# Optimization experiments

Hardware: AMD Instinct MI355X
Metric: run time of the kernel (lower is better)

## Reference

```python
import jax, jax.numpy as jnp
import numpy as np

B, T, C, NH = 8, 512, 512, 8
HD = C // NH

def _layernorm(x, g, b, eps=1e-5):
    mu = jnp.mean(x, axis=-1, keepdims=True)
    var = jnp.var(x, axis=-1, keepdims=True)
    return (x - mu) * jax.lax.rsqrt(var + eps) * g + b

def setup_inputs() -> dict:
    key = jax.random.key(0)
    ks = jax.random.split(key, 5)
    return {
        "x": jax.random.normal(ks[0], (B, T, C), jnp.float32),
        "w_attn": jax.random.normal(ks[1], (3 * C, C), jnp.float32) * (1.0 / np.sqrt(C)),
        "b_attn": jnp.zeros((3 * C,), jnp.float32),
        "w_proj": jax.random.normal(ks[2], (C, C), jnp.float32) * (1.0 / np.sqrt(C)),
        "b_proj": jnp.zeros((C,), jnp.float32),
        "q_gamma": jnp.ones((C,), jnp.float32),
        "q_beta": jnp.zeros((C,), jnp.float32),
        "k_gamma": jnp.ones((C,), jnp.float32),
        "k_beta": jnp.zeros((C,), jnp.float32),
        "rel_emb": jax.random.normal(ks[3], (T, C), jnp.float32) * 0.02,
    }

def reference(x, w_attn, b_attn, w_proj, b_proj, q_gamma, q_beta, k_gamma, k_beta, rel_emb):
    b, t, c = x.shape
    # QKV projection (torch Linear: x @ W.T + b)
    qkv = x @ w_attn.T + b_attn                       # [B,T,3C]
    q, k, v = jnp.split(qkv, 3, axis=-1)
    # per-stream LayerNorm over full embedding dim (q_ln/k_ln = LayerNorm(n_embd))
    q = _layernorm(q, q_gamma, q_beta)
    k = _layernorm(k, k_gamma, k_beta)
    # split heads -> [B,NH,T,HD]
    q = q.reshape(b, t, NH, HD).transpose(0, 2, 1, 3)
    k = k.reshape(b, t, NH, HD).transpose(0, 2, 1, 3)
    v = v.reshape(b, t, NH, HD).transpose(0, 2, 1, 3)
    # relative-position bias: gather rel_emb[|i-j|] -> [T,T,NH,HD]
    idx = jnp.abs(jnp.arange(t)[None, :] - jnp.arange(t)[:, None])  # [T,T] int
    rel = rel_emb[idx].reshape(t, t, NH, HD)
    rel_bias = jnp.einsum("bhqd,qkhd->bhqk", q, rel)  # [B,NH,T,T]
    scale = 1.0 / np.sqrt(HD)
    scores = (jnp.einsum("bhqd,bhkd->bhqk", q, k) + rel_bias) * scale
    causal = jnp.tril(jnp.ones((t, t), bool))
    scores = jnp.where(causal[None, None], scores, jnp.finfo(scores.dtype).min)
    att = jax.nn.softmax(scores, axis=-1)
    y = jnp.einsum("bhqk,bhkd->bhqd", att, v)         # [B,NH,T,HD]
    y = y.transpose(0, 2, 1, 3).reshape(b, t, c)
    return y @ w_proj.T + b_proj
```

## Files before the change

### kernel.cpp

```cpp
#include <hip/hip_runtime.h>
#include <hip/hip_bf16.h>
#include <cstddef>

#define BB 8
#define TT 512
#define CC 512
#define NHH 8
#define HDD 64

typedef __attribute__((ext_vector_type(8))) short short8;
typedef __attribute__((ext_vector_type(4))) float f32x4;

__device__ __forceinline__ unsigned short f2bf(float f) {
    unsigned u = __float_as_uint(f);
    u += 0x7FFFu + ((u >> 16) & 1u);
    return (unsigned short)(u >> 16);
}
__device__ __forceinline__ float bf2f(unsigned short h) {
    return __uint_as_float(((unsigned)h) << 16);
}

__global__ __launch_bounds__(256) void cvt_all_k(
    const float* __restrict__ x, const float* __restrict__ wa,
    const float* __restrict__ wp, const float* __restrict__ rel,
    unsigned short* __restrict__ Xb, unsigned short* __restrict__ Wqb,
    unsigned short* __restrict__ Wpb, unsigned short* __restrict__ Relb)
{
    const int bidx = blockIdx.x;
    const float* in;
    unsigned short* out;
    int base;
    if (bidx < 2048)      { in = x;   out = Xb;   base = bidx; }
    else if (bidx < 2816) { in = wa;  out = Wqb;  base = bidx - 2048; }
    else if (bidx < 3072) { in = wp;  out = Wpb;  base = bidx - 2816; }
    else                  { in = rel; out = Relb; base = bidx - 3072; }
    const int i = base * 1024 + threadIdx.x * 4;
    const float4 v = *(const float4*)(in + i);
    unsigned short tmp[4] = {f2bf(v.x), f2bf(v.y), f2bf(v.z), f2bf(v.w)};
    *(uint2*)(out + i) = *(const uint2*)tmp;
}

__global__ __launch_bounds__(256, 2) void gemm_qkv_mfma(
    const unsigned short* __restrict__ Xb, const unsigned short* __restrict__ Wb,
    const float* __restrict__ bias, unsigned short* __restrict__ qkbuf,
    unsigned short* __restrict__ VT)
{
    __shared__ __align__(16) unsigned short lds[128 * 136];

    const int tid = threadIdx.x;
    const int w = tid >> 6, lane = tid & 63;
    const int c = lane & 15, quad = lane >> 4;
    const int wm = w >> 1, wn = w & 1;
    const int bm = blockIdx.y * 128, bn = blockIdx.x * 128;

    const unsigned short* pp[8];
#pragma unroll
    for (int l = 0; l < 8; ++l) {
        const int ci = w * 8 + l;
        if (ci < 16) {
            const int m16 = ci >> 1, kk = ci & 1;
            pp[l] = Xb + (size_t)(bm + m16 * 16 + c) * 512 + kk * 32 + quad * 8;
        } else {
            const int cb = ci - 16, n16 = cb >> 1, kk = cb & 1;
            pp[l] = Wb + (size_t)(bn + n16 * 16 + c) * 512 + kk * 32 + quad * 8;
        }
    }

    f32x4 acc[4][4];
#pragma unroll
    for (int i = 0; i < 4; ++i)
#pragma unroll
        for (int j = 0; j < 4; ++j) acc[i][j] = (f32x4){0.f, 0.f, 0.f, 0.f};

    short8 pre[8];
#pragma unroll
    for (int l = 0; l < 8; ++l) pre[l] = *(const short8*)pp[l];

    for (int k0 = 0; k0 < 512; k0 += 64) {
        __syncthreads();
#pragma unroll
        for (int l = 0; l < 8; ++l)
            *(short8*)&lds[(w * 8 + l) * 512 + lane * 8] = pre[l];
        __syncthreads();
        if (k0 + 64 < 512) {
#pragma unroll
            for (int l = 0; l < 8; ++l)
                pre[l] = *(const short8*)(pp[l] + k0 + 64);
        }
#pragma unroll
        for (int kk = 0; kk < 2; ++kk) {
            short8 af[4], bfr[4];
#pragma unroll
            for (int i = 0; i < 4; ++i)
                af[i] = *(const short8*)&lds[((wm * 4 + i) * 2 + kk) * 512 + lane * 8];
#pragma unroll
            for (int j = 0; j < 4; ++j)
                bfr[j] = *(const short8*)&lds[(16 + (wn * 4 + j) * 2 + kk) * 512 + lane * 8];
#pragma unroll
            for (int i = 0; i < 4; ++i)
#pragma unroll
                for (int j = 0; j < 4; ++j)
                    acc[i][j] = __builtin_amdgcn_mfma_f32_16x16x32_bf16(
                        af[i], bfr[j], acc[i][j], 0, 0, 0);
        }
    }

    float bj[4];
#pragma unroll
    for (int j = 0; j < 4; ++j) bj[j] = bias[bn + wn * 64 + j * 16 + c];

    if (bn < 1024) {
#pragma unroll
        for (int i = 0; i < 4; ++i)
#pragma unroll
            for (int j = 0; j < 4; ++j) {
                const int n = bn + wn * 64 + j * 16 + c;
#pragma unroll
                for (int r = 0; r < 4; ++r) {
                    const int m = bm + wm * 64 + i * 16 + quad * 4 + r;
                    qkbuf[(size_t)m * 1024 + n] = f2bf(acc[i][j][r] + bj[j]);
                }
            }
    } else {
        __syncthreads();
#pragma unroll
        for (int i = 0; i < 4; ++i)
#pragma unroll
            for (int j = 0; j < 4; ++j) {
                const int col = wn * 64 + j * 16 + c;
                const int row0 = wm * 64 + i * 16 + quad * 4;
                unsigned short t4[4];
#pragma unroll
                for (int r = 0; r < 4; ++r) t4[r] = f2bf(acc[i][j][r] + bj[j]);
                *(uint2*)&lds[col * 136 + row0] = *(const uint2*)t4;
            }
        __syncthreads();
        const int bi = bm >> 9, tb = bm & 511;
        const int hd0 = bn - 1024;
#pragma unroll
        for (int l = 0; l < 8; ++l) {
            const int idx = l * 256 + tid;
            const int col = idx >> 4, grp = idx & 15;
            const short8 v = *(const short8*)&lds[col * 136 + grp * 8];
            const int hd = hd0 + col, h = hd >> 6, d = hd & 63;
            *(short8*)(VT + ((size_t)(bi * NHH + h) * HDD + d) * TT + tb + grp * 8) = v;
        }
    }
}

__global__ __launch_bounds__(256) void ln_k(
    const unsigned short* __restrict__ qkbuf,
    const float* __restrict__ qg, const float* __restrict__ qb,
    const float* __restrict__ kg, const float* __restrict__ kb,
    unsigned short* __restrict__ Qh, unsigned short* __restrict__ Kh)
{
    const int wv = threadIdx.x >> 6, lane = threadIdx.x & 63;
    const int row = blockIdx.x * 4 + wv;
    const int bi = row >> 9, t = row & 511;
    const unsigned short* base = qkbuf + (size_t)row * 1024;

#pragma unroll
    for (int s = 0; s < 2; ++s) {
        const short8 v8 = *(const short8*)(base + s * 512 + lane * 8);
        float vf[8];
#pragma unroll
        for (int i = 0; i < 8; ++i) vf[i] = bf2f(((const unsigned short*)&v8)[i]);
        float sum = 0.f, sq = 0.f;
#pragma unroll
        for (int i = 0; i < 8; ++i) { sum += vf[i]; sq += vf[i] * vf[i]; }
#pragma unroll
        for (int off = 1; off < 64; off <<= 1) {
            sum += __shfl_xor(sum, off);
            sq += __shfl_xor(sq, off);
        }
        const float mu = sum * (1.f / 512.f);
        const float var = sq * (1.f / 512.f) - mu * mu;
        const float rsg = rsqrtf(var + 1e-5f);
        const float* gam = (s ? kg : qg) + lane * 8;
        const float* bet = (s ? kb : qb) + lane * 8;
        const float4 g0 = *(const float4*)gam, g1 = *(const float4*)(gam + 4);
        const float4 b0 = *(const float4*)bet, b1 = *(const float4*)(bet + 4);
        const float gv[8] = {g0.x, g0.y, g0.z, g0.w, g1.x, g1.y, g1.z, g1.w};
        const float bv[8] = {b0.x, b0.y, b0.z, b0.w, b1.x, b1.y, b1.z, b1.w};
        unsigned short o8[8];
#pragma unroll
        for (int i = 0; i < 8; ++i)
            o8[i] = f2bf((vf[i] - mu) * rsg * gv[i] + bv[i]);
        unsigned short* outp = s ? Kh : Qh;
        *(short8*)(outp + ((size_t)(bi * NHH + (lane >> 3)) * TT + t) * HDD
                   + (lane & 7) * 8) = *(const short8*)o8;
    }
}

#define RD_BODY(nr_)                                                            \
    {                                                                           \
        const short8 br0 = *(const short8*)&Rels[((nr_) * 2 + 0) * 512 + lane * 8]; \
        const short8 br1 = *(const short8*)&Rels[((nr_) * 2 + 1) * 512 + lane * 8]; \
        f32x4 a2 = (f32x4){0.f, 0.f, 0.f, 0.f};                                 \
        a2 = __builtin_amdgcn_mfma_f32_16x16x32_bf16(aq0, br0, a2, 0, 0, 0);    \
        a2 = __builtin_amdgcn_mfma_f32_16x16x32_bf16(aq1, br1, a2, 0, 0, 0);    \
        const int colw = (mbase + (nr_) * 16 + c) & 127;                        \
        _Pragma("unroll")                                                       \
        for (int r = 0; r < 4; ++r)                                             \
            RDs[w][(quad * 4 + r) * 132 + colw] = f2bf(a2[r]);                  \
    }

__global__ __launch_bounds__(256, 2) void attn_k(
    const unsigned short* __restrict__ Qh, const unsigned short* __restrict__ Kh,
    const unsigned short* __restrict__ VT, const unsigned short* __restrict__ Relb,
    unsigned short* __restrict__ Yb)
{
    __shared__ __align__(16) unsigned short Qs[8 * 512];
    __shared__ __align__(16) unsigned short Ks[8 * 512];
    __shared__ __align__(16) unsigned short Vs[8 * 512];
    __shared__ __align__(16) unsigned short Rels[16 * 512];
    __shared__ __align__(16) unsigned short Ps[4][16 * 72];
    __shared__ __align__(16) unsigned short RDs[4][16 * 132];

    const int tid = threadIdx.x;
    const int w = tid >> 6;
    const int lane = tid & 63;
    const int c = lane & 15;
    const int quad = lane >> 4;

    const int bid = blockIdx.x;
    const int bit0 = bid & 1, bit8 = (bid >> 8) & 1;
    const int s_ = bit0 ^ bit8;
    const int q0 = (bid >> 1) & 7;
    const int qt = s_ ? 7 - q0 : q0;
    const int h = (bid >> 4) & 7;
    const int b = ((bid >> 7) & 1) | (bit8 << 1) | (bit0 << 2);
    const int i0 = qt * 64;

    const unsigned short* Qbase = Qh + (size_t)(b * NHH + h) * TT * HDD;
    const unsigned short* Kbase = Kh + (size_t)(b * NHH + h) * TT * HDD;
    const unsigned short* Vbase = VT + (size_t)(b * NHH + h) * HDD * TT;
    const unsigned short* Rbase = Relb + h * HDD;

#pragma unroll
    for (int kk = 0; kk < 2; ++kk) {
        const unsigned short* gp =
            Qbase + (size_t)(i0 + w * 16 + c) * HDD + kk * 32 + quad * 8;
        *(short8*)&Qs[(w * 2 + kk) * 512 + lane * 8] = *(const short8*)gp;
    }

    f32x4 oacc[4];
    float m_i[4], l_i[4];
#pragma unroll
    for (int r = 0; r < 4; ++r) { m_i[r] = -1e30f; l_i[r] = 0.f; }
#pragma unroll
    for (int nd = 0; nd < 4; ++nd) oacc[nd] = (f32x4){0.f, 0.f, 0.f, 0.f};

    short8 aq0, aq1;

    for (int jt = 0; jt <= qt; ++jt) {
        const int j0 = jt * 64;
#pragma unroll
        for (int kk = 0; kk < 2; ++kk) {
            const unsigned short* gp =
                Kbase + (size_t)(j0 + w * 16 + c) * HDD + kk * 32 + quad * 8;
            *(short8*)&Ks[(w * 2 + kk) * 512 + lane * 8] = *(const short8*)gp;
        }
#pragma unroll
        for (int js = 0; js < 2; ++js) {
            const unsigned short* gp =
                Vbase + (size_t)(w * 16 + c) * TT + j0 + js * 32 + quad * 8;
            *(short8*)&Vs[(w * 2 + js) * 512 + lane * 8] = *(const short8*)gp;
        }
        const int mbase = i0 - j0 - 63;
        if (jt == 0) {
#pragma unroll
            for (int sb = 0; sb < 2; ++sb) {
#pragma unroll
                for (int kk = 0; kk < 2; ++kk) {
                    const int n16 = w * 2 + sb;
                    int mrow = mbase + n16 * 16 + c;
                    mrow = mrow < 0 ? 0 : (mrow > 511 ? 511 : mrow);
                    *(short8*)&Rels[(n16 * 2 + kk) * 512 + lane * 8] =
                        *(const short8*)(Rbase + (size_t)mrow * CC + kk * 32 + quad * 8);
                }
            }
        } else {
#pragma unroll
            for (int kk = 0; kk < 2; ++kk) {
                int mrow = mbase + w * 16 + c;
                mrow = mrow < 0 ? 0 : (mrow > 511 ? 511 : mrow);
                *(short8*)&Rels[(w * 2 + kk) * 512 + lane * 8] =
                    *(const short8*)(Rbase + (size_t)mrow * CC + kk * 32 + quad * 8);
            }
        }
        __syncthreads();

        if (jt == 0) {
            aq0 = *(const short8*)&Qs[(w * 2 + 0) * 512 + lane * 8];
            aq1 = *(const short8*)&Qs[(w * 2 + 1) * 512 + lane * 8];
        }

        f32x4 sAcc[4];
#pragma unroll
        for (int ns = 0; ns < 4; ++ns) {
            const short8 bk0 = *(const short8*)&Ks[(ns * 2 + 0) * 512 + lane * 8];
            const short8 bk1 = *(const short8*)&Ks[(ns * 2 + 1) * 512 + lane * 8];
            f32x4 a2 = (f32x4){0.f, 0.f, 0.f, 0.f};
            a2 = __builtin_amdgcn_mfma_f32_16x16x32_bf16(aq0, bk0, a2, 0, 0, 0);
            a2 = __builtin_amdgcn_mfma_f32_16x16x32_bf16(aq1, bk1, a2, 0, 0, 0);
            sAcc[ns] = a2;
        }
        if (jt == 0) {
#pragma unroll
            for (int nr = 0; nr < 8; ++nr) RD_BODY(nr)
        } else {
#pragma unroll
            for (int nr = 0; nr < 4; ++nr) RD_BODY(nr)
        }

        const int dbase = i0 - j0;
        float sc[4][4];
#pragma unroll
        for (int ns = 0; ns < 4; ++ns) {
#pragma unroll
            for (int r = 0; r < 4; ++r) {
                const int r16 = quad * 4 + r;
                const int jc = ns * 16 + c;
                const int dp = (dbase + w * 16 + r16 - jc) & 127;
                const float rdv = bf2f(RDs[w][r16 * 132 + dp]);
                const float v = (sAcc[ns][r] + rdv) * 0.125f;
                sc[ns][r] = (j0 + jc > i0 + w * 16 + r16) ? -1e30f : v;
            }
        }
        float alpha[4];
#pragma unroll
        for (int r = 0; r < 4; ++r) {
            float m = fmaxf(fmaxf(sc[0][r], sc[1][r]), fmaxf(sc[2][r], sc[3][r]));
#pragma unroll
            for (int off = 1; off < 16; off <<= 1) m = fmaxf(m, __shfl_xor(m, off));
            const float mn = fmaxf(m_i[r], m);
            alpha[r] = __expf(m_i[r] - mn);
            m_i[r] = mn;
        }
        float rs[4] = {0.f, 0.f, 0.f, 0.f};
#pragma unroll
        for (int ns = 0; ns < 4; ++ns) {
#pragma unroll
            for (int r = 0; r < 4; ++r) {
                const float p = __expf(sc[ns][r] - m_i[r]);
                rs[r] += p;
                Ps[w][(quad * 4 + r) * 72 + ns * 16 + c] = f2bf(p);
            }
        }
#pragma unroll
        for (int r = 0; r < 4; ++r) {
#pragma unroll
            for (int off = 1; off < 16; off <<= 1) rs[r] += __shfl_xor(rs[r], off);
            l_i[r] = l_i[r] * alpha[r] + rs[r];
        }
#pragma unroll
        for (int nd = 0; nd < 4; ++nd)
#pragma unroll
            for (int r = 0; r < 4; ++r) oacc[nd][r] *= alpha[r];

        const short8 ap0 = *(const short8*)&Ps[w][c * 72 + 0 * 32 + quad * 8];
        const short8 ap1 = *(const short8*)&Ps[w][c * 72 + 1 * 32 + quad * 8];
#pragma unroll
        for (int nd = 0; nd < 4; ++nd) {
            const short8 bv0 = *(const short8*)&Vs[(nd * 2 + 0) * 512 + lane * 8];
            const short8 bv1 = *(const short8*)&Vs[(nd * 2 + 1) * 512 + lane * 8];
            oacc[nd] = __builtin_amdgcn_mfma_f32_16x16x32_bf16(ap0, bv0, oacc[nd], 0, 0, 0);
            oacc[nd] = __builtin_amdgcn_mfma_f32_16x16x32_bf16(ap1, bv1, oacc[nd], 0, 0, 0);
        }
        __syncthreads();
    }

#pragma unroll
    for (int r = 0; r < 4; ++r) {
        const float inv = 1.f / l_i[r];
        const int trow = i0 + w * 16 + quad * 4 + r;
        unsigned short* yb = Yb + ((size_t)b * TT + trow) * CC + h * HDD;
#pragma unroll
        for (int nd = 0; nd < 4; ++nd)
            yb[nd * 16 + c] = f2bf(oacc[nd][r] * inv);
    }
}

__global__ __launch_bounds__(256, 2) void gemm_proj_mfma(
    const unsigned short* __restrict__ Yb, const unsigned short* __restrict__ Wp,
    const float* __restrict__ bias, float* __restrict__ out)
{
    __shared__ __align__(16) unsigned short lds[24 * 512];

    const int tid = threadIdx.x;
    const int w = tid >> 6, lane = tid & 63;
    const int c = lane & 15, quad = lane >> 4;
    const int wm = w >> 1, wn = w & 1;
    const int bm = blockIdx.y * 64, bn = blockIdx.x * 128;

    const unsigned short* pp[6];
#pragma unroll
    for (int l = 0; l < 6; ++l) {
        const int ci = w * 6 + l;
        if (ci < 8) {
            const int m16 = ci >> 1, kk = ci & 1;
            pp[l] = Yb + (size_t)(bm + m16 * 16 + c) * 512 + kk * 32 + quad * 8;
        } else {
            const int cb = ci - 8, n16 = cb >> 1, kk = cb & 1;
            pp[l] = Wp + (size_t)(bn + n16 * 16 + c) * 512 + kk * 32 + quad * 8;
        }
    }

    f32x4 acc[2][4];
#pragma unroll
    for (int i = 0; i < 2; ++i)
#pragma unroll
        for (int j = 0; j < 4; ++j) acc[i][j] = (f32x4){0.f, 0.f, 0.f, 0.f};

    short8 pre[6];
#pragma unroll
    for (int l = 0; l < 6; ++l) pre[l] = *(const short8*)pp[l];

    for (int k0 = 0; k0 < 512; k0 += 64) {
        __syncthreads();
#pragma unroll
        for (int l = 0; l < 6; ++l)
            *(short8*)&lds[(w * 6 + l) * 512 + lane * 8] = pre[l];
        __syncthreads();
        if (k0 + 64 < 512) {
#pragma unroll
            for (int l = 0; l < 6; ++l)
                pre[l] = *(const short8*)(pp[l] + k0 + 64);
        }
#pragma unroll
        for (int kk = 0; kk < 2; ++kk) {
            short8 af[2], bfr[4];
#pragma unroll
            for (int i = 0; i < 2; ++i)
                af[i] = *(const short8*)&lds[((wm * 2 + i) * 2 + kk) * 512 + lane * 8];
#pragma unroll
            for (int j = 0; j < 4; ++j)
                bfr[j] = *(const short8*)&lds[(8 + (wn * 4 + j) * 2 + kk) * 512 + lane * 8];
#pragma unroll
            for (int i = 0; i < 2; ++i)
#pragma unroll
                for (int j = 0; j < 4; ++j)
                    acc[i][j] = __builtin_amdgcn_mfma_f32_16x16x32_bf16(
                        af[i], bfr[j], acc[i][j], 0, 0, 0);
        }
    }

#pragma unroll
    for (int j = 0; j < 4; ++j) {
        const int n = bn + wn * 64 + j * 16 + c;
        const float bj = bias[n];
#pragma unroll
        for (int i = 0; i < 2; ++i)
#pragma unroll
            for (int r = 0; r < 4; ++r) {
                const int m = bm + wm * 32 + i * 16 + quad * 4 + r;
                out[(size_t)m * 512 + n] = acc[i][j][r] + bj;
            }
    }
}

extern "C" void kernel_launch(void* const* d_in, const int* in_sizes, int n_in,
                              void* d_out, int out_size, void* d_ws, size_t ws_size,
                              hipStream_t stream)
{
    const float* x      = (const float*)d_in[0];
    const float* w_attn = (const float*)d_in[1];
    const float* b_attn = (const float*)d_in[2];
    const float* w_proj = (const float*)d_in[3];
    const float* b_proj = (const float*)d_in[4];
    const float* q_g    = (const float*)d_in[5];
    const float* q_b    = (const float*)d_in[6];
    const float* k_g    = (const float*)d_in[7];
    const float* k_b    = (const float*)d_in[8];
    const float* rel    = (const float*)d_in[9];
    float* out = (float*)d_out;

    unsigned short* qkbuf = (unsigned short*)d_ws;
    unsigned short* Qh   = qkbuf + (size_t)4096 * 1024;
    unsigned short* Kh   = Qh + (size_t)4096 * 512;
    unsigned short* VT   = Kh + (size_t)4096 * 512;
    unsigned short* Relb = VT + (size_t)4096 * 512;
    unsigned short* Xb   = Relb + (size_t)512 * 512;
    unsigned short* Wqb  = Xb + (size_t)4096 * 512;
    unsigned short* Wpb  = Wqb + (size_t)1536 * 512;
    unsigned short* Yb   = qkbuf;

    cvt_all_k<<<3328, 256, 0, stream>>>(x, w_attn, w_proj, rel, Xb, Wqb, Wpb, Relb);
    gemm_qkv_mfma<<<dim3(12, 32), 256, 0, stream>>>(Xb, Wqb, b_attn, qkbuf, VT);
    ln_k<<<1024, 256, 0, stream>>>(qkbuf, q_g, q_b, k_g, k_b, Qh, Kh);
    attn_k<<<512, 256, 0, stream>>>(Qh, Kh, VT, Relb, Yb);
    gemm_proj_mfma<<<dim3(4, 64), 256, 0, stream>>>(Yb, Wpb, b_proj, out);
}
```

Before: 140.4 us.

## Prefetch next K/V/rel tiles into registers and fold softmax scale into Q

The attention loop now issues global loads for the next K, V and rel-embedding tiles into registers before computing the current tile, then writes them to LDS after the compute. This hides global-memory latency behind the MFMA and softmax work. Q fragments are loaded straight into registers, which drops the Qs LDS buffer. The 1/sqrt(HD) scale moves into the Q LayerNorm output, and the causal mask is applied only on the diagonal tile. In exchange there is higher register pressure with launch bounds of 2 blocks per CU, and two barriers per iteration instead of one.

```diff
diff --git a/kernel.cpp b/kernel.cpp
--- a/kernel.cpp
+++ b/kernel.cpp
@@ -182,10 +182,11 @@
         const float4 b0 = *(const float4*)bet, b1 = *(const float4*)(bet + 4);
         const float gv[8] = {g0.x, g0.y, g0.z, g0.w, g1.x, g1.y, g1.z, g1.w};
         const float bv[8] = {b0.x, b0.y, b0.z, b0.w, b1.x, b1.y, b1.z, b1.w};
+        const float osc = s ? 1.0f : 0.125f;
         unsigned short o8[8];
 #pragma unroll
         for (int i = 0; i < 8; ++i)
-            o8[i] = f2bf((vf[i] - mu) * rsg * gv[i] + bv[i]);
+            o8[i] = f2bf(((vf[i] - mu) * rsg * gv[i] + bv[i]) * osc);
         unsigned short* outp = s ? Kh : Qh;
         *(short8*)(outp + ((size_t)(bi * NHH + (lane >> 3)) * TT + t) * HDD
                    + (lane & 7) * 8) = *(const short8*)o8;
@@ -210,7 +211,6 @@
     const unsigned short* __restrict__ VT, const unsigned short* __restrict__ Relb,
     unsigned short* __restrict__ Yb)
 {
-    __shared__ __align__(16) unsigned short Qs[8 * 512];
     __shared__ __align__(16) unsigned short Ks[8 * 512];
     __shared__ __align__(16) unsigned short Vs[8 * 512];
     __shared__ __align__(16) unsigned short Rels[16 * 512];
@@ -237,11 +237,33 @@
     const unsigned short* Vbase = VT + (size_t)(b * NHH + h) * HDD * TT;
     const unsigned short* Rbase = Relb + h * HDD;
 
+    const unsigned short* qp = Qbase + (size_t)(i0 + w * 16 + c) * HDD + quad * 8;
+    const short8 aq0 = *(const short8*)qp;
+    const short8 aq1 = *(const short8*)(qp + 32);
+
 #pragma unroll
     for (int kk = 0; kk < 2; ++kk) {
-        const unsigned short* gp =
-            Qbase + (size_t)(i0 + w * 16 + c) * HDD + kk * 32 + quad * 8;
-        *(short8*)&Qs[(w * 2 + kk) * 512 + lane * 8] = *(const short8*)gp;
+        const unsigned short* gp = Kbase + (size_t)(w * 16 + c) * HDD + kk * 32 + quad * 8;
+        *(short8*)&Ks[(w * 2 + kk) * 512 + lane * 8] = *(const short8*)gp;
+    }
+#pragma unroll
+    for (int js = 0; js < 2; ++js) {
+        const unsigned short* gp = Vbase + (size_t)(w * 16 + c) * TT + js * 32 + quad * 8;
+        *(short8*)&Vs[(w * 2 + js) * 512 + lane * 8] = *(const short8*)gp;
+    }
+    {
+        const int mb0 = i0 - 63;
+#pragma unroll
+        for (int sb = 0; sb < 2; ++sb) {
+#pragma unroll
+            for (int kk = 0; kk < 2; ++kk) {
+                const int n16 = w * 2 + sb;
+                int mrow = mb0 + n16 * 16 + c;
+                mrow = mrow < 0 ? 0 : (mrow > 511 ? 511 : mrow);
+                *(short8*)&Rels[(n16 * 2 + kk) * 512 + lane * 8] =
+                    *(const short8*)(Rbase + (size_t)mrow * CC + kk * 32 + quad * 8);
+            }
+        }
     }
 
     f32x4 oacc[4];
@@ -251,49 +273,25 @@
 #pragma unroll
     for (int nd = 0; nd < 4; ++nd) oacc[nd] = (f32x4){0.f, 0.f, 0.f, 0.f};
 
-    short8 aq0, aq1;
+    __syncthreads();
 
     for (int jt = 0; jt <= qt; ++jt) {
         const int j0 = jt * 64;
-#pragma unroll
-        for (int kk = 0; kk < 2; ++kk) {
-            const unsigned short* gp =
-                Kbase + (size_t)(j0 + w * 16 + c) * HDD + kk * 32 + quad * 8;
-            *(short8*)&Ks[(w * 2 + kk) * 512 + lane * 8] = *(const short8*)gp;
-        }
-#pragma unroll
-        for (int js = 0; js < 2; ++js) {
-            const unsigned short* gp =
-                Vbase + (size_t)(w * 16 + c) * TT + j0 + js * 32 + quad * 8;
-            *(short8*)&Vs[(w * 2 + js) * 512 + lane * 8] = *(const short8*)gp;
-        }
-        const int mbase = i0 - j0 - 63;
-        if (jt == 0) {
-#pragma unroll
-            for (int sb = 0; sb < 2; ++sb) {
-#pragma unroll
-                for (int kk = 0; kk < 2; ++kk) {
-                    const int n16 = w * 2 + sb;
-                    int mrow = mbase + n16 * 16 + c;
-                    mrow = mrow < 0 ? 0 : (mrow > 511 ? 511 : mrow);
-                    *(short8*)&Rels[(n16 * 2 + kk) * 512 + lane * 8] =
-                        *(const short8*)(Rbase + (size_t)mrow * CC + kk * 32 + quad * 8);
-                }
-            }
-        } else {
-#pragma unroll
-            for (int kk = 0; kk < 2; ++kk) {
-                int mrow = mbase + w * 16 + c;
-                mrow = mrow < 0 ? 0 : (mrow > 511 ? 511 : mrow);
-                *(short8*)&Rels[(w * 2 + kk) * 512 + lane * 8] =
-                    *(const short8*)(Rbase + (size_t)mrow * CC + kk * 32 + quad * 8);
-            }
-        }
-        __syncthreads();
-
-        if (jt == 0) {
-            aq0 = *(const short8*)&Qs[(w * 2 + 0) * 512 + lane * 8];
-            aq1 = *(const short8*)&Qs[(w * 2 + 1) * 512 + lane * 8];
+
+        short8 pK0, pK1, pV0, pV1, pR0, pR1;
+        if (jt < qt) {
+            const int j1 = j0 + 64;
+            const unsigned short* kp = Kbase + (size_t)(j1 + w * 16 + c) * HDD + quad * 8;
+            pK0 = *(const short8*)kp;
+            pK1 = *(const short8*)(kp + 32);
+            const unsigned short* vp = Vbase + (size_t)(w * 16 + c) * TT + j1 + quad * 8;
+            pV0 = *(const short8*)vp;
+            pV1 = *(const short8*)(vp + 32);
+            int mr = i0 - j1 - 63 + w * 16 + c;
+            mr = mr < 0 ? 0 : (mr > 511 ? 511 : mr);
+            const unsigned short* rp = Rbase + (size_t)mr * CC + quad * 8;
+            pR0 = *(const short8*)rp;
+            pR1 = *(const short8*)(rp + 32);
         }
 
         f32x4 sAcc[4];
@@ -306,6 +304,7 @@
             a2 = __builtin_amdgcn_mfma_f32_16x16x32_bf16(aq1, bk1, a2, 0, 0, 0);
             sAcc[ns] = a2;
         }
+        const int mbase = i0 - j0 - 63;
         if (jt == 0) {
 #pragma unroll
             for (int nr = 0; nr < 8; ++nr) RD_BODY(nr)
@@ -324,10 +323,17 @@
                 const int jc = ns * 16 + c;
                 const int dp = (dbase + w * 16 + r16 - jc) & 127;
                 const float rdv = bf2f(RDs[w][r16 * 132 + dp]);
-                const float v = (sAcc[ns][r] + rdv) * 0.125f;
-                sc[ns][r] = (j0 + jc > i0 + w * 16 + r16) ? -1e30f : v;
+                sc[ns][r] = sAcc[ns][r] + rdv;
             }
         }
+        if (jt == qt) {
+#pragma unroll
+            for (int ns = 0; ns < 4; ++ns)
+#pragma unroll
+                for (int r = 0; r < 4; ++r)
+                    if (ns * 16 + c > w * 16 + quad * 4 + r) sc[ns][r] = -1e30f;
+        }
+
         float alpha[4];
 #pragma unroll
         for (int r = 0; r < 4; ++r) {
@@ -368,7 +374,20 @@
             oacc[nd] = __builtin_amdgcn_mfma_f32_16x16x32_bf16(ap0, bv0, oacc[nd], 0, 0, 0);
             oacc[nd] = __builtin_amdgcn_mfma_f32_16x16x32_bf16(ap1, bv1, oacc[nd], 0, 0, 0);
         }
-        __syncthreads();
+
+        if (jt < qt) {
+            __syncthreads();
+#pragma unroll
+            for (int kk = 0; kk < 2; ++kk)
+                *(short8*)&Ks[(w * 2 + kk) * 512 + lane * 8] = (kk ? pK1 : pK0);
+#pragma unroll
+            for (int js = 0; js < 2; ++js)
+                *(short8*)&Vs[(w * 2 + js) * 512 + lane * 8] = (js ? pV1 : pV0);
+#pragma unroll
+            for (int kk = 0; kk < 2; ++kk)
+                *(short8*)&Rels[(w * 2 + kk) * 512 + lane * 8] = (kk ? pR1 : pR0);
+            __syncthreads();
+        }
     }
 
 #pragma unroll
```

Result: no change. 139.5 us (-0.6%).
